# Optimization experiments

Measured on AMD Instinct MI355X. Metric: run time of the kernel, lower is better.

The kernel has to match this reference:

```python
import jax, jax.numpy as jnp
import numpy as np

C = 96          # channels (= output_dim)
NUM_HEADS = 6
DILS = (1, 2, 3)
KS_ATT = 3      # dilate-attention kernel size
KS_COR = 5      # self-correlation kernel size
PAD_COR = 2
LN_EPS = 1e-5


def _unfold(x, k, dil, pad):
    # torch.nn.Unfold(kernel=k, dilation=dil, padding=pad, stride=1)
    # x: [B, C, H, W] -> [B, C, k*k, H, W] (channel-major, kernel row-major)
    B, c, H, W = x.shape
    xp = jnp.pad(x, ((0, 0), (0, 0), (pad, pad), (pad, pad)))
    patches = [xp[:, :, i * dil:i * dil + H, j * dil:j * dil + W]
               for i in range(k) for j in range(k)]
    return jnp.stack(patches, axis=2)


def _layernorm(x, g, b):
    m = jnp.mean(x, axis=-1, keepdims=True)
    v = jnp.mean((x - m) ** 2, axis=-1, keepdims=True)
    return (x - m) * jax.lax.rsqrt(v + LN_EPS) * g + b


def _dilate_attn(q, k, v, dil, head_dim, scale):
    # q,k,v: [B, cb, H, W] with cb = C // num_dilation
    B, cb, H, W = q.shape
    heads = cb // head_dim
    qf = q.reshape(B, heads, head_dim, H * W)                                  # bhdn
    kp = _unfold(k, KS_ATT, dil, dil).reshape(B, heads, head_dim, KS_ATT * KS_ATT, H * W)
    attn = jax.nn.softmax(jnp.einsum('bhdn,bhdkn->bhnk', qf, kp) * scale, axis=-1)
    vp = _unfold(v, KS_ATT, dil, dil).reshape(B, heads, head_dim, KS_ATT * KS_ATT, H * W)
    out = jnp.einsum('bhnk,bhdkn->bnhd', attn, vp)                             # [B,HW,heads,hd]
    return out.reshape(B, H, W, cb)


def _forward(x, g1, b1, Wqkv, bqkv, Wproj, bproj, g2, b2, W1, bm1, W2, bm2):
    B, Cc, H, W = x.shape
    nd = len(DILS)
    head_dim = Cc // NUM_HEADS
    scale = head_dim ** (-0.5)

    xh = jnp.transpose(x, (0, 2, 3, 1))                                        # [B,H,W,C]

    # --- MultiDilatelocalAttention block ---
    y = _layernorm(xh, g1, b1)
    qkv = jnp.einsum('bhwc,oc->bhwo', y, Wqkv) + bqkv                          # 1x1 conv == linear
    qkv = jnp.transpose(qkv, (0, 3, 1, 2)).reshape(B, 3, nd, Cc // nd, H, W)
    outs = []
    for i, d in enumerate(DILS):
        outs.append(_dilate_attn(qkv[:, 0, i], qkv[:, 1, i], qkv[:, 2, i], d, head_dim, scale))
    a = jnp.concatenate(outs, axis=-1)                                         # dilation-major channels
    a = a @ Wproj.T + bproj
    xh = xh + a

    # --- MLP block ---
    z = _layernorm(xh, g2, b2)
    z = jax.nn.gelu(z @ W1.T + bm1, approximate=False) @ W2.T + bm2
    xh = xh + z

    # --- self-correlation ---
    xc = jnp.transpose(xh, (0, 3, 1, 2))                                       # [B,C,H,W]
    xc = jax.nn.relu(xc)
    nrm = jnp.sqrt(jnp.sum(xc * xc, axis=1, keepdims=True))
    xc = xc / jnp.maximum(nrm, 1e-12)                                          # F.normalize dim=1
    pat = _unfold(xc, KS_COR, 1, PAD_COR)                                      # [B,C,25,H,W]
    out = pat.reshape(B, Cc, KS_COR, KS_COR, H, W) * xc[:, :, None, None]
    return jnp.transpose(out, (0, 1, 4, 5, 2, 3))                              # [B,C,H,W,5,5]


def setup_inputs() -> dict:
    key = jax.random.key(0)
    ks = jax.random.split(key, 8)
    B, H, W = 8, 64, 64
    s = 0.02
    return {
        'x': jax.random.normal(ks[0], (B, C, H, W), jnp.float32),
        'g1': jnp.ones((C,), jnp.float32),
        'b1': jnp.zeros((C,), jnp.float32),
        'Wqkv': jax.random.normal(ks[1], (3 * C, C), jnp.float32) * s,
        'bqkv': jnp.zeros((3 * C,), jnp.float32),
        'Wproj': jax.random.normal(ks[2], (C, C), jnp.float32) * s,
        'bproj': jnp.zeros((C,), jnp.float32),
        'g2': jnp.ones((C,), jnp.float32),
        'b2': jnp.zeros((C,), jnp.float32),
        'W1': jax.random.normal(ks[3], (4 * C, C), jnp.float32) * s,
        'bm1': jnp.zeros((4 * C,), jnp.float32),
        'W2': jax.random.normal(ks[4], (C, 4 * C), jnp.float32) * s,
        'bm2': jnp.zeros((C,), jnp.float32),
    }


def reference(x, g1, b1, Wqkv, bqkv, Wproj, bproj, g2, b2, W1, bm1, W2, bm2):
    return _forward(x, g1, b1, Wqkv, bqkv, Wproj, bproj, g2, b2, W1, bm1, W2, bm2)
```

## Files before the change

kernel.cpp:

```cpp
#include <hip/hip_runtime.h>
#include <math.h>

#define NN 4096
#define BN 32768

using short8 = __attribute__((ext_vector_type(8))) short;
using f32x4  = __attribute__((ext_vector_type(4))) float;
typedef unsigned short ushort_t;

__device__ inline unsigned f2bfu(float f) {
    unsigned u = __builtin_bit_cast(unsigned, f);
    u += 0x7FFFu + ((u >> 16) & 1u);
    return u >> 16;
}
__device__ inline ushort_t f2bf(float f) { return (ushort_t)f2bfu(f); }
__device__ inline unsigned pack2(float a, float b) { return f2bfu(a) | (f2bfu(b) << 16); }
__device__ inline float bflo(unsigned u) { return __builtin_bit_cast(float, u << 16); }
__device__ inline float bfhi(unsigned u) { return __builtin_bit_cast(float, u & 0xFFFF0000u); }

__global__ __launch_bounds__(256) void k1_ln_qkv(
    const float* __restrict__ x, const float* __restrict__ g1, const float* __restrict__ b1,
    const float* __restrict__ Wqkv, const float* __restrict__ bqkv,
    unsigned* __restrict__ qkvt32)
{
    __shared__ __align__(16) float    Cs[96 * 69];
    __shared__ __align__(16) ushort_t As[64 * 104];
    __shared__ __align__(16) ushort_t Bs[96 * 104];
    const int tid = threadIdx.x;
    const long bn0 = (long)blockIdx.x * 64;
    const int b = (int)(bn0 >> 12);
    const int n0 = (int)(bn0 & 4095);

    for (int i = 0; i < 24; ++i) {
        int idx = i * 256 + tid;
        int c = idx >> 6, p = idx & 63;
        Cs[c * 69 + p] = x[((long)(b * 96 + c) << 12) + n0 + p];
    }
    __syncthreads();
    {
        int p = tid >> 2, part = tid & 3, c0 = part * 24;
        float s = 0.f, ss = 0.f;
        for (int c = c0; c < c0 + 24; ++c) { float v = Cs[c*69 + p]; s += v; ss += v*v; }
        s  += __shfl_xor(s, 1);  s  += __shfl_xor(s, 2);
        ss += __shfl_xor(ss, 1); ss += __shfl_xor(ss, 2);
        float m = s * (1.f/96.f);
        float rstd = rsqrtf(ss * (1.f/96.f) - m*m + 1e-5f);
        for (int c = c0; c < c0 + 24; ++c)
            Cs[c*69 + p] = (Cs[c*69 + p] - m) * rstd * g1[c] + b1[c];
    }
    __syncthreads();
    for (int i = 0; i < 12; ++i) {
        int idx = i * 256 + tid;
        int p = idx / 48, cp = idx % 48;
        *(unsigned*)&As[p * 104 + 2*cp] = pack2(Cs[(2*cp)*69 + p], Cs[(2*cp+1)*69 + p]);
    }

    const int lane = tid & 63, wv = tid >> 6;
    const int ln = lane & 15, qd = lane >> 4;
    for (int ch = 0; ch < 3; ++ch) {
        __syncthreads();
        for (int i = 0; i < 9; ++i) {
            int idx = i * 256 + tid;
            int o = idx / 24, q4 = idx % 24;
            float4 wvv = *(const float4*)&Wqkv[(long)(ch*96 + o)*96 + q4*4];
            uint2 d; d.x = pack2(wvv.x, wvv.y); d.y = pack2(wvv.z, wvv.w);
            *(uint2*)&Bs[o * 104 + q4*4] = d;
        }
        __syncthreads();
        f32x4 acc[6];
        #pragma unroll
        for (int t = 0; t < 6; ++t) acc[t] = (f32x4){0.f, 0.f, 0.f, 0.f};
        #pragma unroll
        for (int kc = 0; kc < 3; ++kc) {
            short8 a = *(const short8*)&As[(wv*16 + ln)*104 + kc*32 + qd*8];
            #pragma unroll
            for (int t = 0; t < 6; ++t) {
                short8 bf = *(const short8*)&Bs[(t*16 + ln)*104 + kc*32 + qd*8];
                acc[t] = __builtin_amdgcn_mfma_f32_16x16x32_bf16(a, bf, acc[t], 0, 0, 0);
            }
        }
        #pragma unroll
        for (int t = 0; t < 6; ++t)
            #pragma unroll
            for (int r = 0; r < 4; ++r)
                Cs[(t*16 + ln)*69 + (wv*16 + qd*4 + r)] = acc[t][r];
        __syncthreads();
        for (int i = 0; i < 12; ++i) {
            int idx = i * 256 + tid;
            int cp = idx / 64, p = idx % 64;
            int c = 2*cp;
            unsigned d = pack2(Cs[c*69 + p] + bqkv[ch*96 + c],
                               Cs[(c+1)*69 + p] + bqkv[ch*96 + c + 1]);
            qkvt32[((long)(b*144 + ch*48 + cp) << 12) + n0 + p] = d;
        }
    }
}

__global__ __launch_bounds__(256) void k2345(
    const unsigned* __restrict__ qkvt32, const float* __restrict__ x,
    const float* __restrict__ Wproj, const float* __restrict__ bproj,
    const float* __restrict__ g2, const float* __restrict__ b2,
    const float* __restrict__ W1, const float* __restrict__ bm1,
    const float* __restrict__ W2, const float* __restrict__ bm2,
    float* __restrict__ xcn)
{
    __shared__ __align__(16) float    Cs[96 * 69];
    __shared__ __align__(16) ushort_t As[64 * 104];
    __shared__ __align__(16) ushort_t Ah[64 * 104];
    __shared__ __align__(16) ushort_t Bs[96 * 104];
    __shared__ float lnm[64], lnr[64];
    const int tid = threadIdx.x;
    const long bn0 = (long)blockIdx.x * 64;
    const int b = (int)(bn0 >> 12);
    const int n0 = (int)(bn0 & 4095);
    const int h0 = n0 >> 6;
    const int lane = tid & 63, wv = tid >> 6;
    const int ln = lane & 15, qd = lane >> 4;

    for (int it = 0; it < 2; ++it) {
        int item = it * 256 + tid;
        if (item < 384) {
            int p = item & 63;
            int r = item >> 6;
            int head = r & 1, di = r >> 1;
            int dil = di + 1;
            int cp0 = di*16 + head*8;
            const unsigned* Q = qkvt32 + ((long)(b*144 +      cp0) << 12);
            const unsigned* K = qkvt32 + ((long)(b*144 + 48 + cp0) << 12);
            const unsigned* V = qkvt32 + ((long)(b*144 + 96 + cp0) << 12);
            int n = n0 + p, w = p;

            float q[16];
            #pragma unroll
            for (int j = 0; j < 8; ++j) {
                unsigned u = Q[((long)j << 12) + n];
                q[2*j] = bflo(u); q[2*j+1] = bfhi(u);
            }
            float logits[9];
            #pragma unroll
            for (int ki = 0; ki < 3; ++ki)
                #pragma unroll
                for (int kj = 0; kj < 3; ++kj) {
                    int hh = h0 + (ki-1)*dil, ww = w + (kj-1)*dil;
                    float l = 0.f;
                    if ((unsigned)hh < 64u && (unsigned)ww < 64u) {
                        int nn = (hh << 6) + ww;
                        #pragma unroll
                        for (int j = 0; j < 8; ++j) {
                            unsigned u = K[((long)j << 12) + nn];
                            l += q[2*j] * bflo(u) + q[2*j+1] * bfhi(u);
                        }
                    }
                    logits[ki*3 + kj] = l * 0.25f;
                }
            float m = logits[0];
            #pragma unroll
            for (int k = 1; k < 9; ++k) m = fmaxf(m, logits[k]);
            float e[9], s = 0.f;
            #pragma unroll
            for (int k = 0; k < 9; ++k) { e[k] = expf(logits[k] - m); s += e[k]; }
            float inv = 1.f / s;
            float o[16];
            #pragma unroll
            for (int d = 0; d < 16; ++d) o[d] = 0.f;
            #pragma unroll
            for (int ki = 0; ki < 3; ++ki)
                #pragma unroll
                for (int kj = 0; kj < 3; ++kj) {
                    int hh = h0 + (ki-1)*dil, ww = w + (kj-1)*dil;
                    if ((unsigned)hh < 64u && (unsigned)ww < 64u) {
                        int nn = (hh << 6) + ww;
                        float wgt = e[ki*3 + kj] * inv;
                        #pragma unroll
                        for (int j = 0; j < 8; ++j) {
                            unsigned u = V[((long)j << 12) + nn];
                            o[2*j]   += wgt * bflo(u);
                            o[2*j+1] += wgt * bfhi(u);
                        }
                    }
                }
            #pragma unroll
            for (int j = 0; j < 8; ++j)
                *(unsigned*)&As[p * 104 + 2*(cp0 + j)] = pack2(o[2*j], o[2*j+1]);
        }
    }
    for (int i = 0; i < 9; ++i) {
        int idx = i * 256 + tid;
        int o = idx / 24, q4 = idx % 24;
        float4 wvv = *(const float4*)&Wproj[(long)o*96 + q4*4];
        uint2 d; d.x = pack2(wvv.x, wvv.y); d.y = pack2(wvv.z, wvv.w);
        *(uint2*)&Bs[o * 104 + q4*4] = d;
    }
    __syncthreads();
    {
        f32x4 acc[6];
        #pragma unroll
        for (int t = 0; t < 6; ++t) acc[t] = (f32x4){0.f, 0.f, 0.f, 0.f};
        #pragma unroll
        for (int kc = 0; kc < 3; ++kc) {
            short8 a = *(const short8*)&As[(wv*16 + ln)*104 + kc*32 + qd*8];
            #pragma unroll
            for (int t = 0; t < 6; ++t) {
                short8 bf = *(const short8*)&Bs[(t*16 + ln)*104 + kc*32 + qd*8];
                acc[t] = __builtin_amdgcn_mfma_f32_16x16x32_bf16(a, bf, acc[t], 0, 0, 0);
            }
        }
        #pragma unroll
        for (int t = 0; t < 6; ++t)
            #pragma unroll
            for (int r = 0; r < 4; ++r)
                Cs[(t*16 + ln)*69 + (wv*16 + qd*4 + r)] = acc[t][r];
    }
    __syncthreads();
    float resid[24];
    #pragma unroll
    for (int i = 0; i < 24; ++i) {
        int idx = i * 256 + tid;
        int c = idx >> 6, p = idx & 63;
        float v = Cs[c*69 + p] + bproj[c] + x[((long)(b*96 + c) << 12) + n0 + p];
        resid[i] = v;
        Cs[c*69 + p] = v;
    }
    __syncthreads();
    {
        int p = tid >> 2, part = tid & 3, c0 = part * 24;
        float s = 0.f, ss = 0.f;
        for (int c = c0; c < c0 + 24; ++c) { float v = Cs[c*69 + p]; s += v; ss += v*v; }
        s  += __shfl_xor(s, 1);  s  += __shfl_xor(s, 2);
        ss += __shfl_xor(ss, 1); ss += __shfl_xor(ss, 2);
        float m = s * (1.f/96.f);
        float rstd = rsqrtf(ss * (1.f/96.f) - m*m + 1e-5f);
        if (part == 0) { lnm[p] = m; lnr[p] = rstd; }
    }
    __syncthreads();
    for (int i = 0; i < 12; ++i) {
        int idx = i * 256 + tid;
        int p = idx / 48, cp = idx % 48;
        float m = lnm[p], rs = lnr[p];
        int c = 2*cp;
        unsigned d = pack2((Cs[(c  )*69 + p] - m) * rs * g2[c  ] + b2[c  ],
                           (Cs[(c+1)*69 + p] - m) * rs * g2[c+1] + b2[c+1]);
        *(unsigned*)&As[p * 104 + 2*cp] = d;
    }
    f32x4 acc2[6];
    #pragma unroll
    for (int t = 0; t < 6; ++t) acc2[t] = (f32x4){0.f, 0.f, 0.f, 0.f};
    for (int kb = 0; kb < 4; ++kb) {
        __syncthreads();
        for (int i = 0; i < 9; ++i) {
            int idx = i * 256 + tid;
            int o = idx / 24, q4 = idx % 24;
            float4 wvv = *(const float4*)&W1[(long)(kb*96 + o)*96 + q4*4];
            uint2 d; d.x = pack2(wvv.x, wvv.y); d.y = pack2(wvv.z, wvv.w);
            *(uint2*)&Bs[o * 104 + q4*4] = d;
        }
        __syncthreads();
        f32x4 acch[6];
        #pragma unroll
        for (int t = 0; t < 6; ++t) acch[t] = (f32x4){0.f, 0.f, 0.f, 0.f};
        #pragma unroll
        for (int kc = 0; kc < 3; ++kc) {
            short8 a = *(const short8*)&As[(wv*16 + ln)*104 + kc*32 + qd*8];
            #pragma unroll
            for (int t = 0; t < 6; ++t) {
                short8 bf = *(const short8*)&Bs[(t*16 + ln)*104 + kc*32 + qd*8];
                acch[t] = __builtin_amdgcn_mfma_f32_16x16x32_bf16(a, bf, acch[t], 0, 0, 0);
            }
        }
        #pragma unroll
        for (int t = 0; t < 6; ++t) {
            float bias = bm1[kb*96 + t*16 + ln];
            #pragma unroll
            for (int r = 0; r < 4; ++r) {
                float v = acch[t][r] + bias;
                v = 0.5f * v * (1.f + erff(v * 0.70710678118654752f));
                Ah[(wv*16 + qd*4 + r)*104 + t*16 + ln] = f2bf(v);
            }
        }
        __syncthreads();
        for (int i = 0; i < 9; ++i) {
            int idx = i * 256 + tid;
            int o = idx / 24, q4 = idx % 24;
            float4 wvv = *(const float4*)&W2[(long)o*384 + kb*96 + q4*4];
            uint2 d; d.x = pack2(wvv.x, wvv.y); d.y = pack2(wvv.z, wvv.w);
            *(uint2*)&Bs[o * 104 + q4*4] = d;
        }
        __syncthreads();
        #pragma unroll
        for (int kc = 0; kc < 3; ++kc) {
            short8 a = *(const short8*)&Ah[(wv*16 + ln)*104 + kc*32 + qd*8];
            #pragma unroll
            for (int t = 0; t < 6; ++t) {
                short8 bf = *(const short8*)&Bs[(t*16 + ln)*104 + kc*32 + qd*8];
                acc2[t] = __builtin_amdgcn_mfma_f32_16x16x32_bf16(a, bf, acc2[t], 0, 0, 0);
            }
        }
    }
    __syncthreads();
    #pragma unroll
    for (int t = 0; t < 6; ++t)
        #pragma unroll
        for (int r = 0; r < 4; ++r)
            Cs[(t*16 + ln)*69 + (wv*16 + qd*4 + r)] = acc2[t][r];
    __syncthreads();
    #pragma unroll
    for (int i = 0; i < 24; ++i) {
        int idx = i * 256 + tid;
        int c = idx >> 6, p = idx & 63;
        float v = Cs[c*69 + p] + bm2[c] + resid[i];
        Cs[c*69 + p] = fmaxf(v, 0.f);
    }
    __syncthreads();
    {
        int p = tid >> 2, part = tid & 3, c0 = part * 24;
        float ss = 0.f;
        for (int c = c0; c < c0 + 24; ++c) { float v = Cs[c*69 + p]; ss += v*v; }
        ss += __shfl_xor(ss, 1); ss += __shfl_xor(ss, 2);
        if (part == 0) lnr[p] = 1.f / fmaxf(sqrtf(ss), 1e-12f);
    }
    __syncthreads();
    for (int i = 0; i < 12; ++i) {
        int idx = i * 256 + tid;
        int p = idx / 48, cp = idx % 48;
        float inv = lnr[p];
        float2 v = make_float2(Cs[(2*cp)*69 + p] * inv, Cs[(2*cp+1)*69 + p] * inv);
        *(float2*)&xcn[(bn0 + p) * 96 + 2*cp] = v;
    }
}

__global__ __launch_bounds__(256) void k6_selfcorr(
    const float* __restrict__ xcn, float* __restrict__ out)
{
    __shared__ float xt[5 * 20 * 97];
    const int tid = threadIdx.x;
    const int wc = blockIdx.x;
    const int h  = blockIdx.y;
    const int b  = blockIdx.z;
    const int w0 = wc * 16;

    for (int i = 0; i < 38; ++i) {
        int idx = i * 256 + tid;
        if (idx < 9600) {
            int r = idx / (20 * 96);
            int rem = idx - r * (20 * 96);
            int wi = rem / 96, c = rem - wi * 96;
            int hh = h + r - 2, ww = w0 + wi - 2;
            float v = 0.f;
            if ((unsigned)hh < 64u && (unsigned)ww < 64u)
                v = xcn[(((long)b << 12) + (hh << 6) + ww) * 96 + c];
            xt[(r * 20 + wi) * 97 + c] = v;
        }
    }
    __syncthreads();
    f32x4* out4 = (f32x4*)out;
    const long ob4 = (long)b * 2457600 + (long)h * 400 + wc * 100;
    for (int i = 0; i < 38; ++i) {
        int idx = i * 256 + tid;
        if (idx < 9600) {
            int c = idx / 100;
            int r4 = idx - c * 100;
            f32x4 v;
            #pragma unroll
            for (int j = 0; j < 4; ++j) {
                int r = r4 * 4 + j;
                int lw = r / 25, k = r - lw * 25;
                int ki = k / 5, kj = k - ki * 5;
                float center = xt[(42 + lw) * 97 + c];
                float neigh  = xt[(ki * 20 + lw + kj) * 97 + c];
                v[j] = center * neigh;
            }
            __builtin_nontemporal_store(v, &out4[ob4 + (long)c * 25600 + r4]);
        }
    }
}

extern "C" void kernel_launch(void* const* d_in, const int* in_sizes, int n_in,
                              void* d_out, int out_size, void* d_ws, size_t ws_size,
                              hipStream_t stream)
{
    const float* x     = (const float*)d_in[0];
    const float* g1    = (const float*)d_in[1];
    const float* b1    = (const float*)d_in[2];
    const float* Wqkv  = (const float*)d_in[3];
    const float* bqkv  = (const float*)d_in[4];
    const float* Wproj = (const float*)d_in[5];
    const float* bproj = (const float*)d_in[6];
    const float* g2    = (const float*)d_in[7];
    const float* b2    = (const float*)d_in[8];
    const float* W1    = (const float*)d_in[9];
    const float* bm1   = (const float*)d_in[10];
    const float* W2    = (const float*)d_in[11];
    const float* bm2   = (const float*)d_in[12];
    float* out = (float*)d_out;

    char* w = (char*)d_ws;
    unsigned* qkvt32 = (unsigned*)w;  w += (size_t)BN * 288 * 2;
    float*    xcn    = (float*)w;

    k1_ln_qkv  <<<BN / 64, 256, 0, stream>>>(x, g1, b1, Wqkv, bqkv, qkvt32);
    k2345      <<<BN / 64, 256, 0, stream>>>(qkvt32, x, Wproj, bproj, g2, b2,
                                             W1, bm1, W2, bm2, xcn);
    k6_selfcorr<<<dim3(4, 64, 8), 256, 0, stream>>>(xcn, out);
}
```

Before: 436.0 us.

## Compute Q projection inside attention kernel instead of round-tripping through global memory

The first kernel now produces only K and V. The fused attention/MLP kernel reloads x, recomputes LayerNorm, and computes Q for its own 64 pixels with MFMA, keeping Q in shared memory. This removes the global write and read of the Q third of the qkv buffer. The residual x tile is kept in shared memory so the projection and MLP epilogues can add bias and residual straight from the accumulators, dropping extra shared-memory passes and a global reload of x. In exchange, x is read twice and LayerNorm is computed twice, and the second kernel does more work and holds more registers.

```diff
diff --git a/kernel.cpp b/kernel.cpp
--- a/kernel.cpp
+++ b/kernel.cpp
@@ -18,10 +18,10 @@
 __device__ inline float bflo(unsigned u) { return __builtin_bit_cast(float, u << 16); }
 __device__ inline float bfhi(unsigned u) { return __builtin_bit_cast(float, u & 0xFFFF0000u); }
 
-__global__ __launch_bounds__(256) void k1_ln_qkv(
+__global__ __launch_bounds__(256) void k1_ln_kv(
     const float* __restrict__ x, const float* __restrict__ g1, const float* __restrict__ b1,
     const float* __restrict__ Wqkv, const float* __restrict__ bqkv,
-    unsigned* __restrict__ qkvt32)
+    unsigned* __restrict__ kvt32)
 {
     __shared__ __align__(16) float    Cs[96 * 69];
     __shared__ __align__(16) ushort_t As[64 * 104];
@@ -57,12 +57,12 @@
 
     const int lane = tid & 63, wv = tid >> 6;
     const int ln = lane & 15, qd = lane >> 4;
-    for (int ch = 0; ch < 3; ++ch) {
+    for (int kv = 0; kv < 2; ++kv) {
         __syncthreads();
         for (int i = 0; i < 9; ++i) {
             int idx = i * 256 + tid;
             int o = idx / 24, q4 = idx % 24;
-            float4 wvv = *(const float4*)&Wqkv[(long)(ch*96 + o)*96 + q4*4];
+            float4 wvv = *(const float4*)&Wqkv[(long)(96 + kv*96 + o)*96 + q4*4];
             uint2 d; d.x = pack2(wvv.x, wvv.y); d.y = pack2(wvv.z, wvv.w);
             *(uint2*)&Bs[o * 104 + q4*4] = d;
         }
@@ -89,15 +89,17 @@
             int idx = i * 256 + tid;
             int cp = idx / 64, p = idx % 64;
             int c = 2*cp;
-            unsigned d = pack2(Cs[c*69 + p] + bqkv[ch*96 + c],
-                               Cs[(c+1)*69 + p] + bqkv[ch*96 + c + 1]);
-            qkvt32[((long)(b*144 + ch*48 + cp) << 12) + n0 + p] = d;
+            unsigned d = pack2(Cs[c*69 + p] + bqkv[96 + kv*96 + c],
+                               Cs[(c+1)*69 + p] + bqkv[96 + kv*96 + c + 1]);
+            kvt32[((long)(b*96 + kv*48 + cp) << 12) + n0 + p] = d;
         }
     }
 }
 
 __global__ __launch_bounds__(256) void k2345(
-    const unsigned* __restrict__ qkvt32, const float* __restrict__ x,
+    const unsigned* __restrict__ kvt32, const float* __restrict__ x,
+    const float* __restrict__ g1, const float* __restrict__ b1,
+    const float* __restrict__ Wqkv, const float* __restrict__ bqkv,
     const float* __restrict__ Wproj, const float* __restrict__ bproj,
     const float* __restrict__ g2, const float* __restrict__ b2,
     const float* __restrict__ W1, const float* __restrict__ bm1,
@@ -117,6 +119,69 @@
     const int lane = tid & 63, wv = tid >> 6;
     const int ln = lane & 15, qd = lane >> 4;
 
+    for (int i = 0; i < 24; ++i) {
+        int idx = i * 256 + tid;
+        int c = idx >> 6, p = idx & 63;
+        Cs[c * 69 + p] = x[((long)(b * 96 + c) << 12) + n0 + p];
+    }
+    __syncthreads();
+    {
+        int p = tid >> 2, part = tid & 3, c0 = part * 24;
+        float s = 0.f, ss = 0.f;
+        for (int c = c0; c < c0 + 24; ++c) { float v = Cs[c*69 + p]; s += v; ss += v*v; }
+        s  += __shfl_xor(s, 1);  s  += __shfl_xor(s, 2);
+        ss += __shfl_xor(ss, 1); ss += __shfl_xor(ss, 2);
+        float m = s * (1.f/96.f);
+        float rstd = rsqrtf(ss * (1.f/96.f) - m*m + 1e-5f);
+        if (part == 0) { lnm[p] = m; lnr[p] = rstd; }
+    }
+    __syncthreads();
+    for (int i = 0; i < 12; ++i) {
+        int idx = i * 256 + tid;
+        int p = idx / 48, cp = idx % 48;
+        float m = lnm[p], rs = lnr[p];
+        int c = 2*cp;
+        unsigned d = pack2((Cs[(c  )*69 + p] - m) * rs * g1[c  ] + b1[c  ],
+                           (Cs[(c+1)*69 + p] - m) * rs * g1[c+1] + b1[c+1]);
+        *(unsigned*)&As[p * 104 + 2*cp] = d;
+    }
+    for (int i = 0; i < 9; ++i) {
+        int idx = i * 256 + tid;
+        int o = idx / 24, q4 = idx % 24;
+        float4 wvv = *(const float4*)&Wqkv[(long)o*96 + q4*4];
+        uint2 d; d.x = pack2(wvv.x, wvv.y); d.y = pack2(wvv.z, wvv.w);
+        *(uint2*)&Bs[o * 104 + q4*4] = d;
+    }
+    __syncthreads();
+    {
+        f32x4 acc[6];
+        #pragma unroll
+        for (int t = 0; t < 6; ++t) acc[t] = (f32x4){0.f, 0.f, 0.f, 0.f};
+        #pragma unroll
+        for (int kc = 0; kc < 3; ++kc) {
+            short8 a = *(const short8*)&As[(wv*16 + ln)*104 + kc*32 + qd*8];
+            #pragma unroll
+            for (int t = 0; t < 6; ++t) {
+                short8 bf = *(const short8*)&Bs[(t*16 + ln)*104 + kc*32 + qd*8];
+                acc[t] = __builtin_amdgcn_mfma_f32_16x16x32_bf16(a, bf, acc[t], 0, 0, 0);
+            }
+        }
+        #pragma unroll
+        for (int t = 0; t < 6; ++t) {
+            float bias = bqkv[t*16 + ln];
+            #pragma unroll
+            for (int r = 0; r < 4; ++r)
+                Ah[(wv*16 + qd*4 + r)*104 + t*16 + ln] = f2bf(acc[t][r] + bias);
+        }
+    }
+    __syncthreads();
+    for (int i = 0; i < 9; ++i) {
+        int idx = i * 256 + tid;
+        int o = idx / 24, q4 = idx % 24;
+        float4 wvv = *(const float4*)&Wproj[(long)o*96 + q4*4];
+        uint2 d; d.x = pack2(wvv.x, wvv.y); d.y = pack2(wvv.z, wvv.w);
+        *(uint2*)&Bs[o * 104 + q4*4] = d;
+    }
     for (int it = 0; it < 2; ++it) {
         int item = it * 256 + tid;
         if (item < 384) {
@@ -125,15 +190,14 @@
             int head = r & 1, di = r >> 1;
             int dil = di + 1;
             int cp0 = di*16 + head*8;
-            const unsigned* Q = qkvt32 + ((long)(b*144 +      cp0) << 12);
-            const unsigned* K = qkvt32 + ((long)(b*144 + 48 + cp0) << 12);
-            const unsigned* V = qkvt32 + ((long)(b*144 + 96 + cp0) << 12);
-            int n = n0 + p, w = p;
+            const unsigned* K = kvt32 + ((long)(b*96 +      cp0) << 12);
+            const unsigned* V = kvt32 + ((long)(b*96 + 48 + cp0) << 12);
+            int w = p;
 
             float q[16];
             #pragma unroll
             for (int j = 0; j < 8; ++j) {
-                unsigned u = Q[((long)j << 12) + n];
+                unsigned u = *(const unsigned*)&Ah[p * 104 + 2*(cp0 + j)];
                 q[2*j] = bflo(u); q[2*j+1] = bfhi(u);
             }
             float logits[9];
@@ -184,14 +248,8 @@
                 *(unsigned*)&As[p * 104 + 2*(cp0 + j)] = pack2(o[2*j], o[2*j+1]);
         }
     }
-    for (int i = 0; i < 9; ++i) {
-        int idx = i * 256 + tid;
-        int o = idx / 24, q4 = idx % 24;
-        float4 wvv = *(const float4*)&Wproj[(long)o*96 + q4*4];
-        uint2 d; d.x = pack2(wvv.x, wvv.y); d.y = pack2(wvv.z, wvv.w);
-        *(uint2*)&Bs[o * 104 + q4*4] = d;
-    }
-    __syncthreads();
+    __syncthreads();
+    float resid[24];
     {
         f32x4 acc[6];
         #pragma unroll
@@ -206,20 +264,17 @@
             }
         }
         #pragma unroll
-        for (int t = 0; t < 6; ++t)
-            #pragma unroll
-            for (int r = 0; r < 4; ++r)
-                Cs[(t*16 + ln)*69 + (wv*16 + qd*4 + r)] = acc[t][r];
-    }
-    __syncthreads();
-    float resid[24];
-    #pragma unroll
-    for (int i = 0; i < 24; ++i) {
-        int idx = i * 256 + tid;
-        int c = idx >> 6, p = idx & 63;
-        float v = Cs[c*69 + p] + bproj[c] + x[((long)(b*96 + c) << 12) + n0 + p];
-        resid[i] = v;
-        Cs[c*69 + p] = v;
+        for (int t = 0; t < 6; ++t) {
+            int oc = t*16 + ln;
+            float bias = bproj[oc];
+            #pragma unroll
+            for (int r = 0; r < 4; ++r) {
+                int p = wv*16 + qd*4 + r;
+                float v = acc[t][r] + bias + Cs[oc*69 + p];
+                resid[t*4 + r] = v;
+                Cs[oc*69 + p] = v;
+            }
+        }
     }
     __syncthreads();
     {
@@ -298,17 +353,15 @@
     }
     __syncthreads();
     #pragma unroll
-    for (int t = 0; t < 6; ++t)
-        #pragma unroll
-        for (int r = 0; r < 4; ++r)
-            Cs[(t*16 + ln)*69 + (wv*16 + qd*4 + r)] = acc2[t][r];
-    __syncthreads();
-    #pragma unroll
-    for (int i = 0; i < 24; ++i) {
-        int idx = i * 256 + tid;
-        int c = idx >> 6, p = idx & 63;
-        float v = Cs[c*69 + p] + bm2[c] + resid[i];
-        Cs[c*69 + p] = fmaxf(v, 0.f);
+    for (int t = 0; t < 6; ++t) {
+        int oc = t*16 + ln;
+        float bias = bm2[oc];
+        #pragma unroll
+        for (int r = 0; r < 4; ++r) {
+            int p = wv*16 + qd*4 + r;
+            float v = acc2[t][r] + bias + resid[t*4 + r];
+            Cs[oc*69 + p] = fmaxf(v, 0.f);
+        }
     }
     __syncthreads();
     {
@@ -394,11 +447,12 @@
     float* out = (float*)d_out;
 
     char* w = (char*)d_ws;
-    unsigned* qkvt32 = (unsigned*)w;  w += (size_t)BN * 288 * 2;
-    float*    xcn    = (float*)w;
-
-    k1_ln_qkv  <<<BN / 64, 256, 0, stream>>>(x, g1, b1, Wqkv, bqkv, qkvt32);
-    k2345      <<<BN / 64, 256, 0, stream>>>(qkvt32, x, Wproj, bproj, g2, b2,
+    unsigned* kvt32 = (unsigned*)w;  w += (size_t)BN * 192 * 2;
+    float*    xcn   = (float*)w;
+
+    k1_ln_kv   <<<BN / 64, 256, 0, stream>>>(x, g1, b1, Wqkv, bqkv, kvt32);
+    k2345      <<<BN / 64, 256, 0, stream>>>(kvt32, x, g1, b1, Wqkv, bqkv,
+                                             Wproj, bproj, g2, b2,
                                              W1, bm1, W2, bm2, xcn);
     k6_selfcorr<<<dim3(4, 64, 8), 256, 0, stream>>>(xcn, out);
 }
```

New measurement: 421.1 us. 3.4% less time.
